# Kernel tuning notes

Measured on AMD Instinct MI355X. Metric: run time of the kernel, lower is better.

Reference implementation:

```python
import jax, jax.numpy as jnp
import numpy as np

B, S, NV, D = 2, 4096, 8, 256
E = 256          # embedding dim for adaLN conditioning
H = 8            # D / n_head_channels(=32)
HID = 4 * D      # ResLayer MLP hidden
EPS = 1e-5


def setup_inputs() -> dict:
    key = jax.random.key(0)
    ks = jax.random.split(key, 16)
    M = NV * D

    def w(k, shape, scale=0.02):
        return jax.random.normal(k, shape, dtype=jnp.float32) * scale

    mask = jax.random.uniform(ks[0], (B, S, NV)) > 0.2
    mask = mask.at[..., 0].set(True)  # avoid fully-masked rows
    return {
        "x": jax.random.normal(ks[1], (B, S, NV, D), dtype=jnp.float32),
        "emb": jax.random.normal(ks[2], (B, E), dtype=jnp.float32),
        "mask": mask,
        "w_mod1": w(ks[3], (E, 2 * M)), "b_mod1": jnp.zeros((2 * M,), jnp.float32),
        "wq": w(ks[4], (D, D)), "bq": jnp.zeros((D,), jnp.float32),
        "wk": w(ks[5], (D, D)), "bk": jnp.zeros((D,), jnp.float32),
        "wv": w(ks[6], (D, D)), "bv": jnp.zeros((D,), jnp.float32),
        "wo": w(ks[7], (D, D)), "bo": jnp.zeros((D,), jnp.float32),
        "gamma": jnp.full((D,), 1e-6, jnp.float32),
        "w_mod2": w(ks[8], (E, 2 * M)), "b_mod2": jnp.zeros((2 * M,), jnp.float32),
        "w1": w(ks[9], (D, HID)), "b1": jnp.zeros((HID,), jnp.float32),
        "w2": w(ks[10], (HID, D)), "b2": jnp.zeros((D,), jnp.float32),
        "gamma_mlp": jnp.full((D,), 1e-6, jnp.float32),
    }


def _adaln(xin, emb, w, b):
    # AdaptiveLayerNorm over the flattened (NV*D) feature dims,
    # scale/shift conditioned on the embedding.
    b_, s_, nv_, d_ = xin.shape
    xf = xin.reshape(b_, s_, nv_ * d_)
    mu = xf.mean(-1, keepdims=True)
    var = ((xf - mu) ** 2).mean(-1, keepdims=True)
    normed = (xf - mu) * jax.lax.rsqrt(var + EPS)
    scale, shift = jnp.split(emb @ w + b, 2, axis=-1)  # [B, NV*D] each
    out = normed * (1.0 + scale[:, None, :]) + shift[:, None, :]
    return out.reshape(b_, s_, nv_, d_)


def reference(x, emb, mask, w_mod1, b_mod1, wq, bq, wk, bk, wv, bv, wo, bo,
              gamma, w_mod2, b_mod2, w1, b1, w2, b2, gamma_mlp):
    b_, s_, nv_, d_ = x.shape
    hd = d_ // H
    inv_sqrt = jnp.float32(1.0 / np.sqrt(hd))

    # --- attention branch: adaLN -> shape_to_att -> masked attention over variables ---
    h = _adaln(x, emb, w_mod1, b_mod1).reshape(b_ * s_, nv_, d_)
    q = (h @ wq + bq).reshape(b_ * s_, nv_, H, hd)
    k = (h @ wk + bk).reshape(b_ * s_, nv_, H, hd)
    v = (h @ wv + bv).reshape(b_ * s_, nv_, H, hd)
    scores = jnp.einsum('bnhd,bmhd->bhnm', q, k) * inv_sqrt  # [B*S, H, NV, NV]
    mk = mask.reshape(b_ * s_, nv_)
    scores = jnp.where(mk[:, None, None, :], scores, jnp.float32(-1e9))
    attn = jax.nn.softmax(scores, axis=-1)
    o = jnp.einsum('bhnm,bmhd->bnhd', attn, v).reshape(b_ * s_, nv_, d_)
    o = o @ wo + bo
    # dropout is identity at eval; gamma-scaled residual add
    x1 = x + gamma * o.reshape(b_, s_, nv_, d_)

    # --- MLP branch: shape_to_x -> adaLN -> shape_to_att -> ResLayer -> gamma residual ---
    h2 = _adaln(x1, emb, w_mod2, b_mod2)
    m = jax.nn.gelu(h2 @ w1 + b1) @ w2 + b2
    return x1 + gamma_mlp * m
```

## Files before the change

kernel.cpp:

```cpp
#include <hip/hip_runtime.h>
#include <hip/hip_bf16.h>
#include <stdint.h>

#define S_TOK   8192
#define MFEAT   2048

typedef __attribute__((ext_vector_type(4))) float f32x4;
typedef __attribute__((ext_vector_type(8))) short bf16x8;

__device__ __forceinline__ float b2f(uint32_t u) { return __uint_as_float(u << 16); }
__device__ __forceinline__ uint16_t f2b(float f) {
  uint32_t u = __float_as_uint(f);
  uint32_t r = u + 0x7fffu + ((u >> 16) & 1u);
  return (uint16_t)(r >> 16);
}
__device__ __forceinline__ uint32_t pk_bf16(float lo, float hi) {
  uint32_t r;
  asm("v_cvt_pk_bf16_f32 %0, %1, %2" : "=v"(r) : "v"(lo), "v"(hi));
  return r;
}

#define GLP(p) ((__attribute__((address_space(1))) void*)(uintptr_t)(p))
#define LDSP(p) ((__attribute__((address_space(3))) void*)(p))

__global__ __launch_bounds__(256) void k_maskprobe(const uint32_t* __restrict__ m,
                                                   int* __restrict__ flag) {
  __shared__ int s[5];
  const int tid = threadIdx.x;
  if (tid < 5) s[tid] = (tid == 4) ? 0 : 1;
  __syncthreads();
  bool i32ok = true, i8ok = true, f32ok = true, bf16ok = true, saw = false;
  for (int i = tid; i < 1024; i += 256) {
    uint32_t w = m[i];
    if (w > 1u) i32ok = false;
    if (((w | (w >> 8) | (w >> 16) | (w >> 24)) & 0xFEu) != 0) i8ok = false;
    if (w != 0u && w != 0x3F800000u) f32ok = false;
    uint32_t h0 = w & 0xffffu, h1 = w >> 16;
    if ((h0 != 0u && h0 != 0x3F80u) || (h1 != 0u && h1 != 0x3F80u)) bf16ok = false;
    if (w == 0x3F803F80u) saw = true;
  }
  if (!i32ok) s[0] = 0;
  if (!i8ok)  s[1] = 0;
  if (!f32ok) s[2] = 0;
  if (!bf16ok) s[3] = 0;
  if (saw)    s[4] = 1;
  __syncthreads();
  if (tid == 0) {
    int f;
    if (s[0]) f = 0;
    else if (s[1]) f = 1;
    else if (s[3] && s[4]) f = 3;
    else if (s[2]) f = 2;
    else if (s[3]) f = 3;
    else f = 0;
    *flag = f;
  }
}

__global__ __launch_bounds__(256) void k_prep(
    const float* __restrict__ wq, const float* __restrict__ wk,
    const float* __restrict__ wv, const float* __restrict__ wo,
    const float* __restrict__ w1, const float* __restrict__ w2,
    uint16_t* __restrict__ wqf, uint16_t* __restrict__ wof,
    uint16_t* __restrict__ w1f, uint16_t* __restrict__ w2f,
    const void* __restrict__ mask, const int* __restrict__ flag,
    int* __restrict__ mask_i32,
    const float* __restrict__ bq, const float* __restrict__ bk,
    const float* __restrict__ bv, float* __restrict__ biasqkv) {
  int idx = blockIdx.x * 256 + threadIdx.x;
  if (idx < 196608) {
    int o = idx, frag = o >> 9, lane = (o >> 3) & 63, sub = o & 7;
    int ct = frag >> 3, kt = frag & 7;
    int col = ct * 16 + (lane & 15);
    int k = kt * 32 + (lane >> 4) * 8 + sub;
    const float* src = (col < 256) ? wq : (col < 512) ? wk : wv;
    wqf[idx] = f2b(src[k * 256 + (col & 255)]);
  } else if (idx < 262144) {
    int o = idx - 196608, frag = o >> 9, lane = (o >> 3) & 63, sub = o & 7;
    int ct = frag >> 3, kt = frag & 7;
    int col = ct * 16 + (lane & 15);
    int k = kt * 32 + (lane >> 4) * 8 + sub;
    wof[o] = f2b(wo[k * 256 + col]);
  } else if (idx < 524288) {
    int o = idx - 262144, frag = o >> 9, lane = (o >> 3) & 63, sub = o & 7;
    int ct = frag >> 3, kt = frag & 7;
    int col = ct * 16 + (lane & 15);
    int k = kt * 32 + (lane >> 4) * 8 + sub;
    w1f[o] = f2b(w1[k * 1024 + col]);
  } else if (idx < 786432) {
    int o = idx - 524288, frag = o >> 9, lane = (o >> 3) & 63, sub = o & 7;
    int ct = frag >> 5, kt = frag & 31;
    int col = ct * 16 + (lane & 15);
    int k = kt * 32 + (lane >> 4) * 8 + sub;
    w2f[o] = f2b(w2[k * 256 + col]);
  } else if (idx < 851968) {
    int i = idx - 786432;
    int f = *flag;
    int v;
    if (f == 0)      v = ((const int*)mask)[i] != 0;
    else if (f == 1) v = ((const uint8_t*)mask)[i] != 0;
    else if (f == 2) v = ((const uint32_t*)mask)[i] != 0;
    else             v = ((const uint16_t*)mask)[i] != 0;
    mask_i32[i] = v;
  } else if (idx < 852736) {
    int i = idx - 851968;
    biasqkv[i] = (i < 256) ? bq[i] : (i < 512) ? bk[i - 256] : bv[i - 512];
  }
}

__global__ __launch_bounds__(256) void k_mods(
    const float* __restrict__ emb,
    const float* __restrict__ w_mod1, const float* __restrict__ b_mod1,
    const float* __restrict__ w_mod2, const float* __restrict__ b_mod2,
    float* __restrict__ mods) {
  const int j = blockIdx.x * 256 + threadIdx.x;
  const int b = blockIdx.y;
  const int which = blockIdx.z;
  const float* w  = which ? w_mod2 : w_mod1;
  const float* bb = which ? b_mod2 : b_mod1;
  __shared__ float e[256];
  e[threadIdx.x] = emb[b * 256 + threadIdx.x];
  __syncthreads();
  float acc = bb[j];
  for (int kx = 0; kx < 256; kx++) acc += e[kx] * w[(size_t)kx * 4096 + j];
  mods[((size_t)which * 2 + b) * 4096 + j] = acc;
}

__global__ __launch_bounds__(256) void k_qkv(
    const float* __restrict__ x, const float* __restrict__ mods,
    const float* __restrict__ biasqkv, const uint16_t* __restrict__ wqf,
    uint16_t* __restrict__ out, size_t slot, int t0) {
  __shared__ __align__(16) uint16_t As[128 * 256];
  __shared__ float red1[256], red2[256];
  const int tid = threadIdx.x;
  const int l = tid & 63;
  const int wva = tid >> 6;
  const int wr = wva >> 1, wc = wva & 1;
  const int brow = blockIdx.x * 128;
  char* AsB = (char*)As;

  {
    const int r = tid >> 1, ch = (tid & 1) << 7;
    const float4* xp = (const float4*)(x + (size_t)(brow + r) * 256 + ch);
    float s1 = 0.f, s2 = 0.f;
#pragma unroll
    for (int i = 0; i < 32; i++) {
      float4 u = xp[i];
      s1 += u.x + u.y + u.z + u.w;
      s2 += u.x * u.x + u.y * u.y + u.z * u.z + u.w * u.w;
    }
    red1[tid] = s1; red2[tid] = s2;
  }
  __syncthreads();
  {
    const int r = tid >> 1;
    const int base = (r >> 3) << 4;
    float s1 = 0.f, s2 = 0.f;
#pragma unroll
    for (int i = 0; i < 16; i++) { s1 += red1[base + i]; s2 += red2[base + i]; }
    float mean = s1 * (1.f / 2048.f);
    float var = s2 * (1.f / 2048.f) - mean * mean;
    float rs = rsqrtf(var + 1e-5f);
    __syncthreads();
    red1[r] = mean; red2[r] = rs;
  }
  __syncthreads();

#pragma unroll
  for (int it = 0; it < 16; it++) {
    int cidx = it * 256 + tid;
    int row = cidx >> 5, cg = cidx & 31;
    int b = (t0 + ((brow + row) >> 3)) >> 12;
    const float* mo = mods + (size_t)b * 4096 + ((row & 7) << 8) + cg * 8;
    float mean = red1[row], rs = red2[row];
    const float4* xp = (const float4*)(x + (size_t)(brow + row) * 256 + cg * 8);
    float4 u0 = xp[0], u1 = xp[1];
    float4 c0 = *(const float4*)mo,        c1 = *(const float4*)(mo + 4);
    float4 h0 = *(const float4*)(mo + 2048), h1 = *(const float4*)(mo + 2052);
    float v[8] = {u0.x,u0.y,u0.z,u0.w,u1.x,u1.y,u1.z,u1.w};
    float sc[8] = {c0.x,c0.y,c0.z,c0.w,c1.x,c1.y,c1.z,c1.w};
    float sh[8] = {h0.x,h0.y,h0.z,h0.w,h1.x,h1.y,h1.z,h1.w};
    uint32_t w[4];
#pragma unroll
    for (int i = 0; i < 4; i++) {
      float y0 = (v[i*2]   - mean) * rs * (1.f + sc[i*2])   + sh[i*2];
      float y1 = (v[i*2+1] - mean) * rs * (1.f + sc[i*2+1]) + sh[i*2+1];
      w[i] = pk_bf16(y0, y1);
    }
    *(uint4*)(AsB + row * 512 + ((cg * 16) ^ ((row & 7) << 4))) =
        make_uint4(w[0], w[1], w[2], w[3]);
  }
  __syncthreads();

#pragma unroll 1
  for (int nb = 0; nb < 6; nb++) {
    f32x4 acc[4][4];
#pragma unroll
    for (int m = 0; m < 4; m++)
#pragma unroll
      for (int n = 0; n < 4; n++) acc[m][n] = (f32x4)0.f;

#pragma unroll
    for (int kt = 0; kt < 8; kt++) {
      bf16x8 a[4], b[4];
#pragma unroll
      for (int n = 0; n < 4; n++) {
        int ct = nb * 8 + wc * 4 + n;
        b[n] = *(const bf16x8*)(wqf + (((size_t)ct * 8 + kt) * 64 + l) * 8);
      }
#pragma unroll
      for (int m = 0; m < 4; m++) {
        int row = wr * 64 + m * 16 + (l & 15);
        int cb = (kt * 64 + (l >> 4) * 16) ^ ((row & 7) << 4);
        a[m] = *(const bf16x8*)(AsB + row * 512 + cb);
      }
#pragma unroll
      for (int m = 0; m < 4; m++)
#pragma unroll
        for (int n = 0; n < 4; n++)
          acc[m][n] = __builtin_amdgcn_mfma_f32_16x16x32_bf16(a[m], b[n], acc[m][n], 0, 0, 0);
    }

#pragma unroll
    for (int m = 0; m < 4; m++) {
#pragma unroll
      for (int n = 0; n < 4; n++) {
        int col = nb * 128 + wc * 64 + n * 16 + (l & 15);
        float bc = biasqkv[col];
        int b_ = col >> 8, coll = col & 255;
#pragma unroll
        for (int r = 0; r < 4; r++) {
          int row = brow + wr * 64 + m * 16 + (l >> 4) * 4 + r;
          out[(size_t)b_ * slot + (size_t)row * 256 + coll] = f2b(acc[m][n][r] + bc);
        }
      }
    }
  }
}

__global__ __launch_bounds__(256) void k_oproj(
    const uint16_t* __restrict__ A, const uint16_t* __restrict__ wof,
    const float* __restrict__ bias, const float* __restrict__ res,
    const float* __restrict__ gam, float* __restrict__ out,
    float* __restrict__ sbuf) {
  __shared__ __align__(16) uint16_t As[128 * 256];
  __shared__ float sr1[16][2], sr2[16][2];
  const int tid = threadIdx.x;
  const int l = tid & 63;
  const int wva = tid >> 6;
  const int wr = wva >> 1, wc = wva & 1;
  const int brow = blockIdx.x * 128;
  char* AsB = (char*)As;

#pragma unroll
  for (int i = 0; i < 16; i++) {
    int chunk = wva * 16 + i;
    int r = chunk * 2 + (l >> 5);
    int sb = ((l & 31) * 16) ^ ((r & 7) << 4);
    __builtin_amdgcn_global_load_lds(GLP(A + (size_t)(brow + r) * 256 + (sb >> 1)),
                                     LDSP(AsB + chunk * 1024), 16, 0, 0);
  }
  asm volatile("s_waitcnt vmcnt(0)" ::: "memory");
  __syncthreads();

  float ts1[4] = {0.f, 0.f, 0.f, 0.f}, ts2[4] = {0.f, 0.f, 0.f, 0.f};

#pragma unroll 1
  for (int nb = 0; nb < 2; nb++) {
    f32x4 acc[4][4];
#pragma unroll
    for (int m = 0; m < 4; m++)
#pragma unroll
      for (int n = 0; n < 4; n++) acc[m][n] = (f32x4)0.f;

#pragma unroll
    for (int kt = 0; kt < 8; kt++) {
      bf16x8 a[4], b[4];
#pragma unroll
      for (int n = 0; n < 4; n++) {
        int ct = nb * 8 + wc * 4 + n;
        b[n] = *(const bf16x8*)(wof + (((size_t)ct * 8 + kt) * 64 + l) * 8);
      }
#pragma unroll
      for (int m = 0; m < 4; m++) {
        int row = wr * 64 + m * 16 + (l & 15);
        int cb = (kt * 64 + (l >> 4) * 16) ^ ((row & 7) << 4);
        a[m] = *(const bf16x8*)(AsB + row * 512 + cb);
      }
#pragma unroll
      for (int m = 0; m < 4; m++)
#pragma unroll
        for (int n = 0; n < 4; n++)
          acc[m][n] = __builtin_amdgcn_mfma_f32_16x16x32_bf16(a[m], b[n], acc[m][n], 0, 0, 0);
    }

#pragma unroll
    for (int m = 0; m < 4; m++) {
#pragma unroll
      for (int n = 0; n < 4; n++) {
        int col = nb * 128 + wc * 64 + n * 16 + (l & 15);
        float bc = bias[col];
        float gc = gam[col];
#pragma unroll
        for (int r = 0; r < 4; r++) {
          int row = brow + wr * 64 + m * 16 + (l >> 4) * 4 + r;
          float y = res[(size_t)row * 256 + col] + gc * (acc[m][n][r] + bc);
          out[(size_t)row * 256 + col] = y;
          ts1[m] += y; ts2[m] += y * y;
        }
      }
    }
  }

#pragma unroll
  for (int m = 0; m < 4; m++) {
#pragma unroll
    for (int off = 16; off; off >>= 1) {
      ts1[m] += __shfl_xor(ts1[m], off);
      ts2[m] += __shfl_xor(ts2[m], off);
    }
  }
  if ((l & 31) == 0) {
    int h = l >> 5;
#pragma unroll
    for (int m = 0; m < 4; m++) {
      int tok = wr * 8 + 2 * m + h;
      sr1[tok][wc] = ts1[m]; sr2[tok][wc] = ts2[m];
    }
  }
  __syncthreads();
  if (tid < 16) {
    float s1 = sr1[tid][0] + sr1[tid][1];
    float s2 = sr2[tid][0] + sr2[tid][1];
    float mean = s1 * (1.f / 2048.f);
    float var = s2 * (1.f / 2048.f) - mean * mean;
    sbuf[((brow >> 3) + tid) * 2]     = mean;
    sbuf[((brow >> 3) + tid) * 2 + 1] = rsqrtf(var + 1e-5f);
  }
}

__global__ __launch_bounds__(256) void k_mlp(
    float* x1c, const float* __restrict__ mods, const float* __restrict__ sbuf,
    const uint16_t* __restrict__ w1f, const float* __restrict__ b1,
    const uint16_t* __restrict__ w2f, const float* __restrict__ b2,
    const float* __restrict__ gam, int t0) {
  __shared__ __align__(16) uint16_t As[64 * 256];
  __shared__ __align__(16) uint16_t Hs[64 * 128];
  __shared__ float red1[64], red2[64];
  const int tid = threadIdx.x;
  const int l = tid & 63;
  const int w = tid >> 6;
  const int brow = blockIdx.x * 64;
  char* AsB = (char*)As;
  char* HsB = (char*)Hs;

  if (tid < 64) {
    int tok = (brow >> 3) + (tid >> 3);
    red1[tid] = sbuf[tok * 2];
    red2[tid] = sbuf[tok * 2 + 1];
  }
  __syncthreads();

#pragma unroll
  for (int it = 0; it < 8; it++) {
    int cidx = it * 256 + tid;
    int row = cidx >> 5, cg = cidx & 31;
    int b = (t0 + ((brow + row) >> 3)) >> 12;
    const float* mo = mods + (size_t)b * 4096 + ((row & 7) << 8) + cg * 8;
    float mean = red1[row], rs = red2[row];
    const float4* xp = (const float4*)(x1c + (size_t)(brow + row) * 256 + cg * 8);
    float4 u0 = xp[0], u1 = xp[1];
    float4 c0 = *(const float4*)mo,        c1 = *(const float4*)(mo + 4);
    float4 h0 = *(const float4*)(mo + 2048), h1 = *(const float4*)(mo + 2052);
    float v[8] = {u0.x,u0.y,u0.z,u0.w,u1.x,u1.y,u1.z,u1.w};
    float sc[8] = {c0.x,c0.y,c0.z,c0.w,c1.x,c1.y,c1.z,c1.w};
    float sh[8] = {h0.x,h0.y,h0.z,h0.w,h1.x,h1.y,h1.z,h1.w};
    uint32_t wv[4];
#pragma unroll
    for (int i = 0; i < 4; i++) {
      float y0 = (v[i*2]   - mean) * rs * (1.f + sc[i*2])   + sh[i*2];
      float y1 = (v[i*2+1] - mean) * rs * (1.f + sc[i*2+1]) + sh[i*2+1];
      wv[i] = pk_bf16(y0, y1);
    }
    *(uint4*)(AsB + row * 512 + ((cg * 16) ^ ((row & 7) << 4))) =
        make_uint4(wv[0], wv[1], wv[2], wv[3]);
  }

  f32x4 acc2[4][4];
#pragma unroll
  for (int m = 0; m < 4; m++)
#pragma unroll
    for (int n = 0; n < 4; n++) acc2[m][n] = (f32x4)0.f;
  __syncthreads();

#pragma unroll 1
  for (int c = 0; c < 8; c++) {
    f32x4 acc1[2][4];
#pragma unroll
    for (int n = 0; n < 2; n++)
#pragma unroll
      for (int m = 0; m < 4; m++) acc1[n][m] = (f32x4)0.f;
#pragma unroll
    for (int kt = 0; kt < 8; kt++) {
      bf16x8 a[4], b[2];
#pragma unroll
      for (int n = 0; n < 2; n++) {
        int ct = c * 8 + w * 2 + n;
        b[n] = *(const bf16x8*)(w1f + (((size_t)ct * 8 + kt) * 64 + l) * 8);
      }
#pragma unroll
      for (int m = 0; m < 4; m++) {
        int row = m * 16 + (l & 15);
        int cb = (kt * 64 + (l >> 4) * 16) ^ ((row & 7) << 4);
        a[m] = *(const bf16x8*)(AsB + row * 512 + cb);
      }
#pragma unroll
      for (int n = 0; n < 2; n++)
#pragma unroll
        for (int m = 0; m < 4; m++)
          acc1[n][m] = __builtin_amdgcn_mfma_f32_16x16x32_bf16(b[n], a[m], acc1[n][m], 0, 0, 0);
    }
    __syncthreads();
#pragma unroll
    for (int n = 0; n < 2; n++) {
      int hb = w * 32 + n * 16 + (l >> 4) * 4;
      float4 bb = *(const float4*)(b1 + c * 128 + hb);
#pragma unroll
      for (int m = 0; m < 4; m++) {
        int token = m * 16 + (l & 15);
        float g[4];
#pragma unroll
        for (int j = 0; j < 4; j++) {
          float y = acc1[n][m][j] + ((const float*)&bb)[j];
          float t = __expf(-1.702f * y);
          g[j] = __fdividef(y, 1.f + t);
        }
        int byte = (token * 256 + hb * 2) ^ ((token & 7) << 4);
        *(uint2*)(HsB + byte) = make_uint2(pk_bf16(g[0], g[1]), pk_bf16(g[2], g[3]));
      }
    }
    __syncthreads();
#pragma unroll
    for (int kt = 0; kt < 4; kt++) {
      bf16x8 h[4], b[4];
#pragma unroll
      for (int n = 0; n < 4; n++) {
        int ct = w * 4 + n;
        int kidx = c * 4 + kt;
        b[n] = *(const bf16x8*)(w2f + (((size_t)ct * 32 + kidx) * 64 + l) * 8);
      }
#pragma unroll
      for (int m = 0; m < 4; m++) {
        int row = m * 16 + (l & 15);
        int cb = (kt * 64 + (l >> 4) * 16) ^ ((row & 7) << 4);
        h[m] = *(const bf16x8*)(HsB + row * 256 + cb);
      }
#pragma unroll
      for (int m = 0; m < 4; m++)
#pragma unroll
        for (int n = 0; n < 4; n++)
          acc2[m][n] = __builtin_amdgcn_mfma_f32_16x16x32_bf16(h[m], b[n], acc2[m][n], 0, 0, 0);
    }
  }

#pragma unroll
  for (int m = 0; m < 4; m++) {
#pragma unroll
    for (int n = 0; n < 4; n++) {
      int col = w * 64 + n * 16 + (l & 15);
      float bc = b2[col];
      float gc = gam[col];
#pragma unroll
      for (int r = 0; r < 4; r++) {
        int row = brow + m * 16 + (l >> 4) * 4 + r;
        float y = x1c[(size_t)row * 256 + col] + gc * (acc2[m][n][r] + bc);
        x1c[(size_t)row * 256 + col] = y;
      }
    }
  }
}

__global__ __launch_bounds__(256) void k_attn(
    const uint16_t* __restrict__ q, const uint16_t* __restrict__ k,
    const uint16_t* __restrict__ v, const int* __restrict__ mask,
    uint16_t* __restrict__ o) {
  __shared__ __align__(16) uint16_t kk[4][2048];
  __shared__ __align__(16) uint16_t vv[4][2048];
  const int l = threadIdx.x & 63;
  const int wva = threadIdx.x >> 6;
  const int t = blockIdx.x * 4 + wva;

#pragma unroll
  for (int c = 0; c < 4; c++) {
    __builtin_amdgcn_global_load_lds(GLP(k + (size_t)t * 2048 + c * 512 + l * 8),
                                     LDSP(&kk[wva][c * 512]), 16, 0, 0);
    __builtin_amdgcn_global_load_lds(GLP(v + (size_t)t * 2048 + c * 512 + l * 8),
                                     LDSP(&vv[wva][c * 512]), 16, 0, 0);
  }

  const int h = l >> 3, n = l & 7;
  const uint4* qp = (const uint4*)(q + (size_t)t * 2048 + n * 256 + h * 32);
  float qf[32];
#pragma unroll
  for (int c = 0; c < 4; c++) {
    uint4 u = qp[c];
    qf[c*8+0]=b2f(u.x & 0xffff); qf[c*8+1]=b2f(u.x >> 16);
    qf[c*8+2]=b2f(u.y & 0xffff); qf[c*8+3]=b2f(u.y >> 16);
    qf[c*8+4]=b2f(u.z & 0xffff); qf[c*8+5]=b2f(u.z >> 16);
    qf[c*8+6]=b2f(u.w & 0xffff); qf[c*8+7]=b2f(u.w >> 16);
  }
  asm volatile("s_waitcnt vmcnt(0)" ::: "memory");

  float s[8];
#pragma unroll
  for (int m = 0; m < 8; m++) {
    const uint4* kp = (const uint4*)&kk[wva][m * 256 + h * 32];
    float acc = 0.f;
#pragma unroll
    for (int c = 0; c < 4; c++) {
      uint4 u = kp[c];
      acc += qf[c*8+0]*b2f(u.x & 0xffff) + qf[c*8+1]*b2f(u.x >> 16)
           + qf[c*8+2]*b2f(u.y & 0xffff) + qf[c*8+3]*b2f(u.y >> 16)
           + qf[c*8+4]*b2f(u.z & 0xffff) + qf[c*8+5]*b2f(u.z >> 16)
           + qf[c*8+6]*b2f(u.w & 0xffff) + qf[c*8+7]*b2f(u.w >> 16);
    }
    s[m] = acc * 0.17677669529663687f;
  }
  const int* mk = mask + (size_t)t * 8;
  float mx = -1e30f;
#pragma unroll
  for (int m = 0; m < 8; m++) { s[m] = mk[m] ? s[m] : -1e9f; mx = fmaxf(mx, s[m]); }
  float p[8], sum = 0.f;
#pragma unroll
  for (int m = 0; m < 8; m++) { p[m] = __expf(s[m] - mx); sum += p[m]; }
  float inv = __fdividef(1.f, sum);
  float of[32];
#pragma unroll
  for (int d = 0; d < 32; d++) of[d] = 0.f;
#pragma unroll
  for (int m = 0; m < 8; m++) {
    float pm = p[m] * inv;
    const uint4* vp = (const uint4*)&vv[wva][m * 256 + h * 32];
#pragma unroll
    for (int c = 0; c < 4; c++) {
      uint4 u = vp[c];
      of[c*8+0]+=pm*b2f(u.x & 0xffff); of[c*8+1]+=pm*b2f(u.x >> 16);
      of[c*8+2]+=pm*b2f(u.y & 0xffff); of[c*8+3]+=pm*b2f(u.y >> 16);
      of[c*8+4]+=pm*b2f(u.z & 0xffff); of[c*8+5]+=pm*b2f(u.z >> 16);
      of[c*8+6]+=pm*b2f(u.w & 0xffff); of[c*8+7]+=pm*b2f(u.w >> 16);
    }
  }
  uint16_t* op = o + (size_t)t * 2048 + n * 256 + h * 32;
#pragma unroll
  for (int c = 0; c < 4; c++) {
    ((uint4*)op)[c] = make_uint4(pk_bf16(of[c*8+0], of[c*8+1]),
                                 pk_bf16(of[c*8+2], of[c*8+3]),
                                 pk_bf16(of[c*8+4], of[c*8+5]),
                                 pk_bf16(of[c*8+6], of[c*8+7]));
  }
}

extern "C" void kernel_launch(void* const* d_in, const int* in_sizes, int n_in,
                              void* d_out, int out_size, void* d_ws, size_t ws_size,
                              hipStream_t stream) {
  const float* x      = (const float*)d_in[0];
  const float* emb    = (const float*)d_in[1];
  const void*  mask   = d_in[2];
  const float* w_mod1 = (const float*)d_in[3];
  const float* b_mod1 = (const float*)d_in[4];
  const float* wq = (const float*)d_in[5];
  const float* bq = (const float*)d_in[6];
  const float* wk = (const float*)d_in[7];
  const float* bk = (const float*)d_in[8];
  const float* wv = (const float*)d_in[9];
  const float* bv = (const float*)d_in[10];
  const float* wo = (const float*)d_in[11];
  const float* bo = (const float*)d_in[12];
  const float* gamma     = (const float*)d_in[13];
  const float* w_mod2    = (const float*)d_in[14];
  const float* b_mod2    = (const float*)d_in[15];
  const float* w1 = (const float*)d_in[16];
  const float* b1 = (const float*)d_in[17];
  const float* w2 = (const float*)d_in[18];
  const float* b2 = (const float*)d_in[19];
  const float* gamma_mlp = (const float*)d_in[20];

  char* ws = (char*)d_ws;
  float*    mods = (float*)ws;
  uint16_t* wqf = (uint16_t*)(ws + 65536);
  uint16_t* wof = wqf + 196608;
  uint16_t* w1f = wof + 65536;
  uint16_t* w2f = w1f + 262144;
  int*      mask_i32 = (int*)(w2f + 262144);
  int*      flag = mask_i32 + 65536;
  float*    biasqkv = (float*)(flag + 1);
  float*    sbuf = biasqkv + 768;
  uint16_t* slots = (uint16_t*)(ws + (2u << 20));
  float*    xout = (float*)d_out;

  size_t budget = (ws_size > (3u << 20)) ? ws_size - (2u << 20) : 0;
  int maxtok = (int)(budget / 16384);
  int chunk_tokens = 16;
  for (int c = 8192; c >= 16; c >>= 1) { if (c <= maxtok) { chunk_tokens = c; break; } }
  const int nchunks = S_TOK / chunk_tokens;
  const int crows = chunk_tokens * 8;
  const size_t slot = (size_t)crows * 256;
  uint16_t* C0 = slots;
  uint16_t* C1 = C0 + slot;

  k_maskprobe<<<dim3(1), 256, 0, stream>>>((const uint32_t*)mask, flag);
  k_prep<<<dim3(3331), 256, 0, stream>>>(wq, wk, wv, wo, w1, w2, wqf, wof, w1f, w2f,
                                         mask, flag, mask_i32, bq, bk, bv, biasqkv);
  k_mods<<<dim3(16, 2, 2), 256, 0, stream>>>(emb, w_mod1, b_mod1, w_mod2, b_mod2, mods);

  for (int c = 0; c < nchunks; c++) {
    const int t0 = c * chunk_tokens;
    const size_t eo = (size_t)t0 * MFEAT;
    const float* xc = x + eo;
    float* x1c = xout + eo;
    k_qkv<<<dim3(crows / 128), 256, 0, stream>>>(xc, mods, biasqkv, wqf, C1, slot, t0);
    k_attn<<<dim3(chunk_tokens / 4), 256, 0, stream>>>(C1, C1 + slot, C1 + 2 * slot,
                                                       mask_i32 + (size_t)t0 * 8, C0);
    k_oproj<<<dim3(crows / 128), 256, 0, stream>>>(C0, wof, bo, xc, gamma, x1c, sbuf);
    k_mlp<<<dim3(crows / 64), 256, 0, stream>>>(x1c, mods + 2 * 4096, sbuf, w1f, b1,
                                                w2f, b2, gamma_mlp, t0);
  }
}
```

Baseline: 314.9 us.

## Fuse output projection and LayerNorm stats into the MLP kernel

```diff
diff --git a/kernel.cpp b/kernel.cpp
--- a/kernel.cpp
+++ b/kernel.cpp
@@ -238,115 +238,16 @@
   }
 }
 
-__global__ __launch_bounds__(256) void k_oproj(
-    const uint16_t* __restrict__ A, const uint16_t* __restrict__ wof,
-    const float* __restrict__ bias, const float* __restrict__ res,
-    const float* __restrict__ gam, float* __restrict__ out,
-    float* __restrict__ sbuf) {
-  __shared__ __align__(16) uint16_t As[128 * 256];
-  __shared__ float sr1[16][2], sr2[16][2];
-  const int tid = threadIdx.x;
-  const int l = tid & 63;
-  const int wva = tid >> 6;
-  const int wr = wva >> 1, wc = wva & 1;
-  const int brow = blockIdx.x * 128;
-  char* AsB = (char*)As;
-
-#pragma unroll
-  for (int i = 0; i < 16; i++) {
-    int chunk = wva * 16 + i;
-    int r = chunk * 2 + (l >> 5);
-    int sb = ((l & 31) * 16) ^ ((r & 7) << 4);
-    __builtin_amdgcn_global_load_lds(GLP(A + (size_t)(brow + r) * 256 + (sb >> 1)),
-                                     LDSP(AsB + chunk * 1024), 16, 0, 0);
-  }
-  asm volatile("s_waitcnt vmcnt(0)" ::: "memory");
-  __syncthreads();
-
-  float ts1[4] = {0.f, 0.f, 0.f, 0.f}, ts2[4] = {0.f, 0.f, 0.f, 0.f};
-
-#pragma unroll 1
-  for (int nb = 0; nb < 2; nb++) {
-    f32x4 acc[4][4];
-#pragma unroll
-    for (int m = 0; m < 4; m++)
-#pragma unroll
-      for (int n = 0; n < 4; n++) acc[m][n] = (f32x4)0.f;
-
-#pragma unroll
-    for (int kt = 0; kt < 8; kt++) {
-      bf16x8 a[4], b[4];
-#pragma unroll
-      for (int n = 0; n < 4; n++) {
-        int ct = nb * 8 + wc * 4 + n;
-        b[n] = *(const bf16x8*)(wof + (((size_t)ct * 8 + kt) * 64 + l) * 8);
-      }
-#pragma unroll
-      for (int m = 0; m < 4; m++) {
-        int row = wr * 64 + m * 16 + (l & 15);
-        int cb = (kt * 64 + (l >> 4) * 16) ^ ((row & 7) << 4);
-        a[m] = *(const bf16x8*)(AsB + row * 512 + cb);
-      }
-#pragma unroll
-      for (int m = 0; m < 4; m++)
-#pragma unroll
-        for (int n = 0; n < 4; n++)
-          acc[m][n] = __builtin_amdgcn_mfma_f32_16x16x32_bf16(a[m], b[n], acc[m][n], 0, 0, 0);
-    }
-
-#pragma unroll
-    for (int m = 0; m < 4; m++) {
-#pragma unroll
-      for (int n = 0; n < 4; n++) {
-        int col = nb * 128 + wc * 64 + n * 16 + (l & 15);
-        float bc = bias[col];
-        float gc = gam[col];
-#pragma unroll
-        for (int r = 0; r < 4; r++) {
-          int row = brow + wr * 64 + m * 16 + (l >> 4) * 4 + r;
-          float y = res[(size_t)row * 256 + col] + gc * (acc[m][n][r] + bc);
-          out[(size_t)row * 256 + col] = y;
-          ts1[m] += y; ts2[m] += y * y;
-        }
-      }
-    }
-  }
-
-#pragma unroll
-  for (int m = 0; m < 4; m++) {
-#pragma unroll
-    for (int off = 16; off; off >>= 1) {
-      ts1[m] += __shfl_xor(ts1[m], off);
-      ts2[m] += __shfl_xor(ts2[m], off);
-    }
-  }
-  if ((l & 31) == 0) {
-    int h = l >> 5;
-#pragma unroll
-    for (int m = 0; m < 4; m++) {
-      int tok = wr * 8 + 2 * m + h;
-      sr1[tok][wc] = ts1[m]; sr2[tok][wc] = ts2[m];
-    }
-  }
-  __syncthreads();
-  if (tid < 16) {
-    float s1 = sr1[tid][0] + sr1[tid][1];
-    float s2 = sr2[tid][0] + sr2[tid][1];
-    float mean = s1 * (1.f / 2048.f);
-    float var = s2 * (1.f / 2048.f) - mean * mean;
-    sbuf[((brow >> 3) + tid) * 2]     = mean;
-    sbuf[((brow >> 3) + tid) * 2 + 1] = rsqrtf(var + 1e-5f);
-  }
-}
-
-__global__ __launch_bounds__(256) void k_mlp(
-    float* x1c, const float* __restrict__ mods, const float* __restrict__ sbuf,
+__global__ __launch_bounds__(256) void k_tail(
+    const uint16_t* __restrict__ A , const uint16_t* __restrict__ wof,
+    const float* __restrict__ bo, const float* __restrict__ x,
+    const float* __restrict__ gamma, const float* __restrict__ mods2,
     const uint16_t* __restrict__ w1f, const float* __restrict__ b1,
     const uint16_t* __restrict__ w2f, const float* __restrict__ b2,
-    const float* __restrict__ gam, int t0) {
+    const float* __restrict__ gam2, float* x1c, int t0) {
   __shared__ __align__(16) uint16_t As[64 * 256];
   __shared__ __align__(16) uint16_t Hs[64 * 128];
-  __shared__ float red1[64], red2[64];
+  __shared__ float sr1[8][4], sr2[8][4], mean_s[8], rs_s[8];
   const int tid = threadIdx.x;
   const int l = tid & 63;
   const int w = tid >> 6;
@@ -354,10 +255,87 @@
   char* AsB = (char*)As;
   char* HsB = (char*)Hs;
 
-  if (tid < 64) {
-    int tok = (brow >> 3) + (tid >> 3);
-    red1[tid] = sbuf[tok * 2];
-    red2[tid] = sbuf[tok * 2 + 1];
+#pragma unroll
+  for (int i = 0; i < 8; i++) {
+    int chunk = w * 8 + i;
+    int r = chunk * 2 + (l >> 5);
+    int sb = ((l & 31) * 16) ^ ((r & 7) << 4);
+    __builtin_amdgcn_global_load_lds(GLP(A + (size_t)(brow + r) * 256 + (sb >> 1)),
+                                     LDSP(AsB + chunk * 1024), 16, 0, 0);
+  }
+  asm volatile("s_waitcnt vmcnt(0)" ::: "memory");
+  __syncthreads();
+
+  float ts1[4] = {0.f, 0.f, 0.f, 0.f}, ts2[4] = {0.f, 0.f, 0.f, 0.f};
+#pragma unroll 1
+  for (int nb = 0; nb < 2; nb++) {
+    f32x4 acc[4][2];
+#pragma unroll
+    for (int m = 0; m < 4; m++) { acc[m][0] = (f32x4)0.f; acc[m][1] = (f32x4)0.f; }
+    __builtin_amdgcn_s_setprio(1);
+#pragma unroll
+    for (int kt = 0; kt < 8; kt++) {
+      bf16x8 a[4], b[2];
+#pragma unroll
+      for (int n = 0; n < 2; n++) {
+        int ct = w * 4 + nb * 2 + n;
+        b[n] = *(const bf16x8*)(wof + (((size_t)ct * 8 + kt) * 64 + l) * 8);
+      }
+#pragma unroll
+      for (int m = 0; m < 4; m++) {
+        int row = m * 16 + (l & 15);
+        int cb = (kt * 64 + (l >> 4) * 16) ^ ((row & 7) << 4);
+        a[m] = *(const bf16x8*)(AsB + row * 512 + cb);
+      }
+#pragma unroll
+      for (int m = 0; m < 4; m++)
+#pragma unroll
+        for (int n = 0; n < 2; n++)
+          acc[m][n] = __builtin_amdgcn_mfma_f32_16x16x32_bf16(a[m], b[n], acc[m][n], 0, 0, 0);
+    }
+    __builtin_amdgcn_s_setprio(0);
+#pragma unroll
+    for (int m = 0; m < 4; m++) {
+#pragma unroll
+      for (int n = 0; n < 2; n++) {
+        int col = w * 64 + nb * 32 + n * 16 + (l & 15);
+        float bc = bo[col];
+        float gc = gamma[col];
+#pragma unroll
+        for (int r = 0; r < 4; r++) {
+          int row = brow + m * 16 + (l >> 4) * 4 + r;
+          float y = x[(size_t)row * 256 + col] + gc * (acc[m][n][r] + bc);
+          x1c[(size_t)row * 256 + col] = y;
+          ts1[m] += y; ts2[m] += y * y;
+        }
+      }
+    }
+  }
+
+#pragma unroll
+  for (int m = 0; m < 4; m++) {
+#pragma unroll
+    for (int off = 16; off; off >>= 1) {
+      ts1[m] += __shfl_xor(ts1[m], off);
+      ts2[m] += __shfl_xor(ts2[m], off);
+    }
+  }
+  if ((l & 31) == 0) {
+    int h = l >> 5;
+#pragma unroll
+    for (int m = 0; m < 4; m++) {
+      int tok = 2 * m + h;
+      sr1[tok][w] = ts1[m]; sr2[tok][w] = ts2[m];
+    }
+  }
+  __syncthreads();
+  if (tid < 8) {
+    float s1 = sr1[tid][0] + sr1[tid][1] + sr1[tid][2] + sr1[tid][3];
+    float s2 = sr2[tid][0] + sr2[tid][1] + sr2[tid][2] + sr2[tid][3];
+    float mean = s1 * (1.f / 2048.f);
+    float var = s2 * (1.f / 2048.f) - mean * mean;
+    mean_s[tid] = mean;
+    rs_s[tid] = rsqrtf(var + 1e-5f);
   }
   __syncthreads();
 
@@ -366,8 +344,8 @@
     int cidx = it * 256 + tid;
     int row = cidx >> 5, cg = cidx & 31;
     int b = (t0 + ((brow + row) >> 3)) >> 12;
-    const float* mo = mods + (size_t)b * 4096 + ((row & 7) << 8) + cg * 8;
-    float mean = red1[row], rs = red2[row];
+    const float* mo = mods2 + (size_t)b * 4096 + ((row & 7) << 8) + cg * 8;
+    float mean = mean_s[row >> 3], rs = rs_s[row >> 3];
     const float4* xp = (const float4*)(x1c + (size_t)(brow + row) * 256 + cg * 8);
     float4 u0 = xp[0], u1 = xp[1];
     float4 c0 = *(const float4*)mo,        c1 = *(const float4*)(mo + 4);
@@ -400,6 +378,7 @@
     for (int n = 0; n < 2; n++)
 #pragma unroll
       for (int m = 0; m < 4; m++) acc1[n][m] = (f32x4)0.f;
+    __builtin_amdgcn_s_setprio(1);
 #pragma unroll
     for (int kt = 0; kt < 8; kt++) {
       bf16x8 a[4], b[2];
@@ -420,6 +399,7 @@
         for (int m = 0; m < 4; m++)
           acc1[n][m] = __builtin_amdgcn_mfma_f32_16x16x32_bf16(b[n], a[m], acc1[n][m], 0, 0, 0);
     }
+    __builtin_amdgcn_s_setprio(0);
     __syncthreads();
 #pragma unroll
     for (int n = 0; n < 2; n++) {
@@ -440,6 +420,7 @@
       }
     }
     __syncthreads();
+    __builtin_amdgcn_s_setprio(1);
 #pragma unroll
     for (int kt = 0; kt < 4; kt++) {
       bf16x8 h[4], b[4];
@@ -461,6 +442,7 @@
         for (int n = 0; n < 4; n++)
           acc2[m][n] = __builtin_amdgcn_mfma_f32_16x16x32_bf16(h[m], b[n], acc2[m][n], 0, 0, 0);
     }
+    __builtin_amdgcn_s_setprio(0);
   }
 
 #pragma unroll
@@ -469,7 +451,7 @@
     for (int n = 0; n < 4; n++) {
       int col = w * 64 + n * 16 + (l & 15);
       float bc = b2[col];
-      float gc = gam[col];
+      float gc = gam2[col];
 #pragma unroll
       for (int r = 0; r < 4; r++) {
         int row = brow + m * 16 + (l >> 4) * 4 + r;
@@ -594,7 +576,6 @@
   int*      mask_i32 = (int*)(w2f + 262144);
   int*      flag = mask_i32 + 65536;
   float*    biasqkv = (float*)(flag + 1);
-  float*    sbuf = biasqkv + 768;
   uint16_t* slots = (uint16_t*)(ws + (2u << 20));
   float*    xout = (float*)d_out;
 
@@ -621,8 +602,8 @@
     k_qkv<<<dim3(crows / 128), 256, 0, stream>>>(xc, mods, biasqkv, wqf, C1, slot, t0);
     k_attn<<<dim3(chunk_tokens / 4), 256, 0, stream>>>(C1, C1 + slot, C1 + 2 * slot,
                                                        mask_i32 + (size_t)t0 * 8, C0);
-    k_oproj<<<dim3(crows / 128), 256, 0, stream>>>(C0, wof, bo, xc, gamma, x1c, sbuf);
-    k_mlp<<<dim3(crows / 64), 256, 0, stream>>>(x1c, mods + 2 * 4096, sbuf, w1f, b1,
-                                                w2f, b2, gamma_mlp, t0);
-  }
-}
+    k_tail<<<dim3(crows / 64), 256, 0, stream>>>(C0, wof, bo, xc, gamma,
+                                                 mods + 2 * 4096, w1f, b1, w2f, b2,
+                                                 gamma_mlp, x1c, t0);
+  }
+}
```

Result: slower. 379.9 us (+20.6%).

## Halve MLP hidden chunk width and drop LDS stats staging in k_mlp

Applied to the files above, without the earlier changes.

```diff
diff --git a/kernel.cpp b/kernel.cpp
--- a/kernel.cpp
+++ b/kernel.cpp
@@ -345,8 +345,7 @@
     const uint16_t* __restrict__ w2f, const float* __restrict__ b2,
     const float* __restrict__ gam, int t0) {
   __shared__ __align__(16) uint16_t As[64 * 256];
-  __shared__ __align__(16) uint16_t Hs[64 * 128];
-  __shared__ float red1[64], red2[64];
+  __shared__ __align__(16) uint16_t Hs[64 * 64];
   const int tid = threadIdx.x;
   const int l = tid & 63;
   const int w = tid >> 6;
@@ -354,20 +353,14 @@
   char* AsB = (char*)As;
   char* HsB = (char*)Hs;
 
-  if (tid < 64) {
-    int tok = (brow >> 3) + (tid >> 3);
-    red1[tid] = sbuf[tok * 2];
-    red2[tid] = sbuf[tok * 2 + 1];
-  }
-  __syncthreads();
-
 #pragma unroll
   for (int it = 0; it < 8; it++) {
     int cidx = it * 256 + tid;
     int row = cidx >> 5, cg = cidx & 31;
-    int b = (t0 + ((brow + row) >> 3)) >> 12;
+    int gtok = (brow + row) >> 3;
+    int b = (t0 + gtok) >> 12;
     const float* mo = mods + (size_t)b * 4096 + ((row & 7) << 8) + cg * 8;
-    float mean = red1[row], rs = red2[row];
+    float mean = sbuf[gtok * 2], rs = sbuf[gtok * 2 + 1];
     const float4* xp = (const float4*)(x1c + (size_t)(brow + row) * 256 + cg * 8);
     float4 u0 = xp[0], u1 = xp[1];
     float4 c0 = *(const float4*)mo,        c1 = *(const float4*)(mo + 4);
@@ -394,66 +387,55 @@
   __syncthreads();
 
 #pragma unroll 1
-  for (int c = 0; c < 8; c++) {
-    f32x4 acc1[2][4];
-#pragma unroll
-    for (int n = 0; n < 2; n++)
-#pragma unroll
-      for (int m = 0; m < 4; m++) acc1[n][m] = (f32x4)0.f;
+  for (int c = 0; c < 16; c++) {
+    f32x4 acc1[4];
+#pragma unroll
+    for (int m = 0; m < 4; m++) acc1[m] = (f32x4)0.f;
 #pragma unroll
     for (int kt = 0; kt < 8; kt++) {
-      bf16x8 a[4], b[2];
-#pragma unroll
-      for (int n = 0; n < 2; n++) {
-        int ct = c * 8 + w * 2 + n;
-        b[n] = *(const bf16x8*)(w1f + (((size_t)ct * 8 + kt) * 64 + l) * 8);
-      }
+      int ct = c * 4 + w;
+      bf16x8 bw = *(const bf16x8*)(w1f + (((size_t)ct * 8 + kt) * 64 + l) * 8);
 #pragma unroll
       for (int m = 0; m < 4; m++) {
         int row = m * 16 + (l & 15);
         int cb = (kt * 64 + (l >> 4) * 16) ^ ((row & 7) << 4);
-        a[m] = *(const bf16x8*)(AsB + row * 512 + cb);
-      }
-#pragma unroll
-      for (int n = 0; n < 2; n++)
-#pragma unroll
-        for (int m = 0; m < 4; m++)
-          acc1[n][m] = __builtin_amdgcn_mfma_f32_16x16x32_bf16(b[n], a[m], acc1[n][m], 0, 0, 0);
+        bf16x8 a = *(const bf16x8*)(AsB + row * 512 + cb);
+        acc1[m] = __builtin_amdgcn_mfma_f32_16x16x32_bf16(bw, a, acc1[m], 0, 0, 0);
+      }
     }
     __syncthreads();
-#pragma unroll
-    for (int n = 0; n < 2; n++) {
-      int hb = w * 32 + n * 16 + (l >> 4) * 4;
-      float4 bb = *(const float4*)(b1 + c * 128 + hb);
+    {
+      int hb = w * 16 + (l >> 4) * 4;
+      float4 bb = *(const float4*)(b1 + c * 64 + hb);
 #pragma unroll
       for (int m = 0; m < 4; m++) {
         int token = m * 16 + (l & 15);
         float g[4];
 #pragma unroll
         for (int j = 0; j < 4; j++) {
-          float y = acc1[n][m][j] + ((const float*)&bb)[j];
+          float y = acc1[m][j] + ((const float*)&bb)[j];
           float t = __expf(-1.702f * y);
           g[j] = __fdividef(y, 1.f + t);
         }
-        int byte = (token * 256 + hb * 2) ^ ((token & 7) << 4);
+        int byte = (token * 128 + hb * 2) ^ ((token & 7) << 4);
         *(uint2*)(HsB + byte) = make_uint2(pk_bf16(g[0], g[1]), pk_bf16(g[2], g[3]));
       }
     }
     __syncthreads();
 #pragma unroll
-    for (int kt = 0; kt < 4; kt++) {
+    for (int kt = 0; kt < 2; kt++) {
       bf16x8 h[4], b[4];
 #pragma unroll
       for (int n = 0; n < 4; n++) {
         int ct = w * 4 + n;
-        int kidx = c * 4 + kt;
+        int kidx = c * 2 + kt;
         b[n] = *(const bf16x8*)(w2f + (((size_t)ct * 32 + kidx) * 64 + l) * 8);
       }
 #pragma unroll
       for (int m = 0; m < 4; m++) {
         int row = m * 16 + (l & 15);
         int cb = (kt * 64 + (l >> 4) * 16) ^ ((row & 7) << 4);
-        h[m] = *(const bf16x8*)(HsB + row * 256 + cb);
+        h[m] = *(const bf16x8*)(HsB + row * 128 + cb);
       }
 #pragma unroll
       for (int m = 0; m < 4; m++)
```

After: 372.5 us. 1.18x slower.
